# Optimization experiments

Hardware: AMD Instinct MI355X
Metric: run time of the kernel (lower is better)

Reference implementation:

```python
import jax, jax.numpy as jnp
import numpy as np

B, N, M = 2, 2048, 2048
Q_DIM = 1024
HEADS = 8
DIM_HEAD = 64
INNER = HEADS * DIM_HEAD  # 512


def setup_inputs() -> dict:
    key = jax.random.key(0)
    ks = jax.random.split(key, 7)
    s_in = 1.0 / np.sqrt(Q_DIM)
    s_out = 1.0 / np.sqrt(INNER)
    return {
        "x": jax.random.normal(ks[0], (B, N, Q_DIM), dtype=jnp.float32),
        "context": jax.random.normal(ks[1], (B, M, Q_DIM), dtype=jnp.float32),
        "Wq": jax.random.normal(ks[2], (Q_DIM, INNER), dtype=jnp.float32) * s_in,
        "Wk": jax.random.normal(ks[3], (Q_DIM, INNER), dtype=jnp.float32) * s_in,
        "Wv": jax.random.normal(ks[4], (Q_DIM, INNER), dtype=jnp.float32) * s_in,
        "Wo": jax.random.normal(ks[5], (INNER, Q_DIM), dtype=jnp.float32) * s_out,
        "bo": jax.random.normal(ks[6], (Q_DIM,), dtype=jnp.float32) * 0.01,
    }


def reference(x, context, Wq, Wk, Wv, Wo, bo):
    scale = DIM_HEAD ** (-0.5)
    # projections, split heads: [b, n, inner] -> [b, h, n, d]
    def split_heads(t):
        b, n, _ = t.shape
        return t.reshape(b, n, HEADS, DIM_HEAD).transpose(0, 2, 1, 3)
    q = split_heads(x @ Wq)
    k = split_heads(context @ Wk)
    v = split_heads(context @ Wv)
    sim = jnp.einsum('bhid,bhjd->bhij', q, k) * scale  # [b,h,n,m] full score matrix
    attn = jax.nn.softmax(sim, axis=-1)
    out = jnp.einsum('bhij,bhjd->bhid', attn, v)       # [b,h,n,d]
    out = out.transpose(0, 2, 1, 3).reshape(x.shape[0], x.shape[1], INNER)
    return out @ Wo + bo
```

## Files before the change

kernel.cpp:

```cpp
#include <hip/hip_runtime.h>

typedef __attribute__((ext_vector_type(8))) short short8;
typedef __attribute__((ext_vector_type(4))) short bf16x4;
typedef __attribute__((ext_vector_type(4))) float floatx4;
typedef __attribute__((ext_vector_type(4))) float f32x4;

__device__ __forceinline__ short f2bf(float f) {
    union { float f; unsigned u; } v;
    v.f = f;
    unsigned r = v.u + 0x7fffu + ((v.u >> 16) & 1u);
    return (short)(r >> 16);
}
__device__ __forceinline__ short8 cvt8(f32x4 a, f32x4 b) {
    short8 r;
    r[0] = f2bf(a[0]); r[1] = f2bf(a[1]); r[2] = f2bf(a[2]); r[3] = f2bf(a[3]);
    r[4] = f2bf(b[0]); r[5] = f2bf(b[1]); r[6] = f2bf(b[2]); r[7] = f2bf(b[3]);
    return r;
}
__device__ __forceinline__ bf16x4 pack4(float a, float b, float c, float d) {
    union { float f; unsigned u; } x;
    unsigned ua, ub, uc, ud;
    x.f = a; ua = (x.u + 0x8000u) >> 16;
    x.f = b; ub = (x.u + 0x8000u) >> 16;
    x.f = c; uc = (x.u + 0x8000u) >> 16;
    x.f = d; ud = (x.u + 0x8000u) >> 16;
    union { bf16x4 s; unsigned u2[2]; } r;
    r.u2[0] = ua | (ub << 16);
    r.u2[1] = uc | (ud << 16);
    return r.s;
}

#define MFMA_BF16(a, b, c) __builtin_amdgcn_mfma_f32_16x16x32_bf16((a), (b), (c), 0, 0, 0)

__device__ __forceinline__ floatx4 mfma16(bf16x4 a, bf16x4 b, floatx4 c) {
#if __has_builtin(__builtin_amdgcn_mfma_f32_16x16x16bf16_1k)
    return __builtin_amdgcn_mfma_f32_16x16x16bf16_1k(a, b, c, 0, 0, 0);
#else
    floatx4 d;
    asm volatile("v_mfma_f32_16x16x16_bf16 %0, %1, %2, %3"
                 : "=&v"(d) : "v"(a), "v"(b), "v"(c));
    return d;
#endif
}

__device__ __forceinline__ float fast_exp2(float x) {
#if __has_builtin(__builtin_amdgcn_exp2f)
    return __builtin_amdgcn_exp2f(x);
#else
    return exp2f(x);
#endif
}

#define QSCALE_LOG2E 0.18033688011112042f

__global__ __launch_bounds__(256) void cvt_f32_bf16(const float* __restrict__ x,
                                                    const float* __restrict__ ctx,
                                                    short* __restrict__ xb,
                                                    short* __restrict__ ctxb) {
    const size_t i = ((size_t)blockIdx.x * 256 + threadIdx.x) * 8;
    const size_t NT = (size_t)4096 * 1024;
    const float* src = (i < NT) ? x : ctx;
    short* dst = (i < NT) ? xb : ctxb;
    const size_t j = (i < NT) ? i : i - NT;
    f32x4 a = *(const f32x4*)(src + j);
    f32x4 b = *(const f32x4*)(src + j + 4);
    *(short8*)(dst + j) = cvt8(a, b);
}

__global__ __launch_bounds__(256) void transpose_all(const float* __restrict__ Wq,
                                                     const float* __restrict__ Wk,
                                                     const float* __restrict__ Wv,
                                                     const float* __restrict__ Wo,
                                                     short* __restrict__ WqT,
                                                     short* __restrict__ WkT,
                                                     short* __restrict__ WvT,
                                                     short* __restrict__ WoT) {
    const int z = blockIdx.z;
    const float* src = (z == 0) ? Wq : (z == 1) ? Wk : (z == 2) ? Wv : Wo;
    short* dst = (z == 0) ? WqT : (z == 1) ? WkT : (z == 2) ? WvT : WoT;
    const int R = (z < 3) ? 1024 : 512;
    const int C = (z < 3) ? 512 : 1024;
    const int c0 = blockIdx.x * 32;
    const int r0 = blockIdx.y * 32;
    if (c0 >= C || r0 >= R) return;
    __shared__ float tile[32][33];
    const int tx = threadIdx.x;
    const int ty = threadIdx.y;
#pragma unroll
    for (int i = 0; i < 32; i += 8)
        tile[ty + i][tx] = src[(r0 + ty + i) * C + c0 + tx];
    __syncthreads();
#pragma unroll
    for (int i = 0; i < 32; i += 8)
        dst[(c0 + ty + i) * R + r0 + tx] = f2bf(tile[tx][ty + i]);
}

__global__ __launch_bounds__(256, 4) void gemm_qkv(const short* __restrict__ xb,
                                                   const short* __restrict__ ctxb,
                                                   const short* __restrict__ WqT,
                                                   const short* __restrict__ WkT,
                                                   const short* __restrict__ WvT,
                                                   short* __restrict__ Qw,
                                                   short* __restrict__ Kw,
                                                   short* __restrict__ Vtw) {
    const int z = blockIdx.z;
    const short* A  = (z == 0) ? xb : ctxb;
    const short* WT = (z == 0) ? WqT : (z == 1) ? WkT : WvT;
    const int tid = threadIdx.x;
    const int w = tid >> 6;
    const int lane = tid & 63;
    const int quad = lane >> 4, ln = lane & 15;
    const int wr = w >> 1, wc = w & 1;
    const int row0 = blockIdx.x * 64;
    const int col0 = blockIdx.y * 128;

    __shared__ __align__(16) short Alds[2][64][32];
    __shared__ __align__(16) short Blds[2][128][32];

    const int srow = tid >> 2;
    const int scol = (tid & 3) * 8;
    const short* aG = A + (size_t)(row0 + srow) * 1024 + scol;
    const short* bG0 = WT + (size_t)(col0 + srow) * 1024 + scol;
    const short* bG1 = WT + (size_t)(col0 + srow + 64) * 1024 + scol;

    floatx4 acc[2][4] = {};

    {
        *(short8*)(&Alds[0][srow][scol]) = *(const short8*)(aG);
        *(short8*)(&Blds[0][srow][scol]) = *(const short8*)(bG0);
        *(short8*)(&Blds[0][srow + 64][scol]) = *(const short8*)(bG1);
    }
    __syncthreads();

    const int nsteps = 1024 / 32;
    for (int it = 0; it < nsteps; ++it) {
        short8 ar, br0, br1;
        const bool more = (it + 1 < nsteps);
        if (more) {
            const int kk = (it + 1) * 32;
            ar  = *(const short8*)(aG + kk);
            br0 = *(const short8*)(bG0 + kk);
            br1 = *(const short8*)(bG1 + kk);
        }
        const int b = it & 1;
        short8 af[2], bf4[4];
#pragma unroll
        for (int i = 0; i < 2; ++i)
            af[i] = *(const short8*)(&Alds[b][wr * 32 + i * 16 + ln][quad * 8]);
#pragma unroll
        for (int t = 0; t < 4; ++t)
            bf4[t] = *(const short8*)(&Blds[b][wc * 64 + t * 16 + ln][quad * 8]);
#pragma unroll
        for (int i = 0; i < 2; ++i)
#pragma unroll
            for (int t = 0; t < 4; ++t)
                acc[i][t] = MFMA_BF16(af[i], bf4[t], acc[i][t]);
        if (more) {
            const int nb = (it + 1) & 1;
            *(short8*)(&Alds[nb][srow][scol]) = ar;
            *(short8*)(&Blds[nb][srow][scol]) = br0;
            *(short8*)(&Blds[nb][srow + 64][scol]) = br1;
        }
        __syncthreads();
    }

    const float oscale = (z == 0) ? QSCALE_LOG2E : 1.0f;
    short* dst = (z == 0) ? Qw : (z == 1) ? Kw : Vtw;
#pragma unroll
    for (int i = 0; i < 2; ++i)
#pragma unroll
        for (int t = 0; t < 4; ++t)
#pragma unroll
            for (int r = 0; r < 4; ++r) {
                const int R = row0 + wr * 32 + i * 16 + quad * 4 + r;
                const int C = col0 + wc * 64 + t * 16 + ln;
                const int b = R >> 11, n = R & 2047;
                const int h = C >> 6, d = C & 63;
                const short val = f2bf(acc[i][t][r] * oscale);
                if (z < 2)
                    dst[((b * 8 + h) * 2048 + n) * 64 + d] = val;
                else
                    dst[((b * 8 + h) * 64 + d) * 2048 + n] = val;
            }
}

__global__ __launch_bounds__(256, 3) void attn_kernel(const short* __restrict__ Q,
                                                      const short* __restrict__ K,
                                                      const short* __restrict__ Vt,
                                                      float* __restrict__ Opart,
                                                      float* __restrict__ lbuf,
                                                      int chunkLen) {
    const int tid = threadIdx.x;
    const int w = tid >> 6;
    const int lane = tid & 63;
    const int quad = lane >> 4;
    const int ln = lane & 15;
    const int q0 = blockIdx.x * 64;
    const int bh = blockIdx.y;
    const int c = blockIdx.z;

    __shared__ __align__(16) short klds[2][64][72];
    __shared__ __align__(16) short vlds[2][64][72];

    const short* Qbh = Q + bh * 2048 * 64;
    const short* Kbh = K + bh * 2048 * 64;
    const short* Vbh = Vt + bh * 64 * 2048;

    short8 qf[2];
    {
        const int qrow = q0 + w * 16 + ln;
        qf[0] = *(const short8*)(Qbh + qrow * 64 + quad * 8);
        qf[1] = *(const short8*)(Qbh + qrow * 64 + 32 + quad * 8);
    }

    floatx4 ot[4] = {};
    float lp = 0.f;

    const int sr = tid >> 3;
    const int sc = (tid & 7) * 8;

    auto computeTile = [&](int b) {
        short8 kf[8];
#pragma unroll
        for (int t = 0; t < 4; ++t)
#pragma unroll
            for (int ks = 0; ks < 2; ++ks)
                kf[t * 2 + ks] = *(const short8*)(&klds[b][t * 16 + ln][ks * 32 + quad * 8]);
        bf16x4 vf[16];
#pragma unroll
        for (int dt = 0; dt < 4; ++dt)
#pragma unroll
            for (int t = 0; t < 4; ++t)
                vf[dt * 4 + t] = *(const bf16x4*)(&vlds[b][dt * 16 + ln][t * 16 + quad * 4]);

        floatx4 s[4] = {};
#pragma unroll
        for (int ks = 0; ks < 2; ++ks)
#pragma unroll
            for (int t = 0; t < 4; ++t)
                s[t] = MFMA_BF16(kf[t * 2 + ks], qf[ks], s[t]);

        bf16x4 pf[4];
#pragma unroll
        for (int t = 0; t < 4; ++t) {
            float p0 = fast_exp2(s[t][0]);
            float p1 = fast_exp2(s[t][1]);
            float p2 = fast_exp2(s[t][2]);
            float p3 = fast_exp2(s[t][3]);
            lp += (p0 + p1) + (p2 + p3);
            pf[t] = pack4(p0, p1, p2, p3);
        }
#pragma unroll
        for (int t = 0; t < 4; ++t)
#pragma unroll
            for (int dt = 0; dt < 4; ++dt)
                ot[dt] = mfma16(vf[dt * 4 + t], pf[t], ot[dt]);
    };

    const int j0s = c * chunkLen;
    const int nt = chunkLen >> 6;

    {
        short8 k0 = *(const short8*)(Kbh + j0s * 64 + tid * 8);
        short8 k1 = *(const short8*)(Kbh + j0s * 64 + (tid + 256) * 8);
        short8 v0 = *(const short8*)(Vbh + sr * 2048 + j0s + sc);
        short8 v1 = *(const short8*)(Vbh + (sr + 32) * 2048 + j0s + sc);
        *(short8*)(&klds[0][sr][sc]) = k0;
        *(short8*)(&klds[0][sr + 32][sc]) = k1;
        *(short8*)(&vlds[0][sr][sc]) = v0;
        *(short8*)(&vlds[0][sr + 32][sc]) = v1;
    }
    __syncthreads();

    for (int it = 0; it < nt; ++it) {
        short8 k0, k1, v0, v1;
        const bool more = (it + 1 < nt);
        if (more) {
            const int jn = j0s + (it + 1) * 64;
            k0 = *(const short8*)(Kbh + jn * 64 + tid * 8);
            k1 = *(const short8*)(Kbh + jn * 64 + (tid + 256) * 8);
            v0 = *(const short8*)(Vbh + sr * 2048 + jn + sc);
            v1 = *(const short8*)(Vbh + (sr + 32) * 2048 + jn + sc);
        }
        computeTile(it & 1);
        if (more) {
            const int nb = (it + 1) & 1;
            *(short8*)(&klds[nb][sr][sc]) = k0;
            *(short8*)(&klds[nb][sr + 32][sc]) = k1;
            *(short8*)(&vlds[nb][sr][sc]) = v0;
            *(short8*)(&vlds[nb][sr + 32][sc]) = v1;
        }
        __syncthreads();
    }

    lp += __shfl_xor(lp, 16);
    lp += __shfl_xor(lp, 32);

    const int n = q0 + w * 16 + ln;
    float* obase = Opart + (((size_t)(c * 16 + bh) * 2048 + n) * 64) + quad * 4;
#pragma unroll
    for (int dt = 0; dt < 4; ++dt)
        *(f32x4*)(obase + dt * 16) = ot[dt];
    if (quad == 0)
        lbuf[(size_t)(c * 16 + bh) * 2048 + n] = lp;
}

__global__ __launch_bounds__(256) void combine_kernel(const float* __restrict__ Opart,
                                                      const float* __restrict__ lbuf,
                                                      short* __restrict__ Aw,
                                                      int nchunks) {
    const int d = threadIdx.x;
    const int rid = blockIdx.x * 4 + threadIdx.y;
    const int bh = rid >> 11, n = rid & 2047;

    float L = 0.f, O = 0.f;
    for (int c = 0; c < nchunks; ++c) {
        L += lbuf[(size_t)(c * 16 + bh) * 2048 + n];
        O += Opart[(((size_t)(c * 16 + bh) * 2048 + n) * 64) + d];
    }
    const int b = bh >> 3, h = bh & 7;
    Aw[((size_t)(b * 2048 + n) * 512) + h * 64 + d] = f2bf(O / L);
}

__global__ __launch_bounds__(256, 4) void gemm_final(const short* __restrict__ A,
                                                     const short* __restrict__ WoT,
                                                     const float* __restrict__ bias,
                                                     float* __restrict__ out) {
    const int tid = threadIdx.x;
    const int w = tid >> 6;
    const int lane = tid & 63;
    const int quad = lane >> 4, ln = lane & 15;
    const int wr = w >> 1, wc = w & 1;
    const int row0 = blockIdx.x * 64;
    const int col0 = blockIdx.y * 128;

    __shared__ __align__(16) short Alds[2][64][32];
    __shared__ __align__(16) short Blds[2][128][32];

    const int srow = tid >> 2;
    const int scol = (tid & 3) * 8;
    const short* aG = A + (size_t)(row0 + srow) * 512 + scol;
    const short* bG0 = WoT + (size_t)(col0 + srow) * 512 + scol;
    const short* bG1 = WoT + (size_t)(col0 + srow + 64) * 512 + scol;

    floatx4 acc[2][4] = {};

    {
        *(short8*)(&Alds[0][srow][scol]) = *(const short8*)(aG);
        *(short8*)(&Blds[0][srow][scol]) = *(const short8*)(bG0);
        *(short8*)(&Blds[0][srow + 64][scol]) = *(const short8*)(bG1);
    }
    __syncthreads();

    const int nsteps = 512 / 32;
    for (int it = 0; it < nsteps; ++it) {
        short8 ar, br0, br1;
        const bool more = (it + 1 < nsteps);
        if (more) {
            const int kk = (it + 1) * 32;
            ar  = *(const short8*)(aG + kk);
            br0 = *(const short8*)(bG0 + kk);
            br1 = *(const short8*)(bG1 + kk);
        }
        const int b = it & 1;
        short8 af[2], bf4[4];
#pragma unroll
        for (int i = 0; i < 2; ++i)
            af[i] = *(const short8*)(&Alds[b][wr * 32 + i * 16 + ln][quad * 8]);
#pragma unroll
        for (int t = 0; t < 4; ++t)
            bf4[t] = *(const short8*)(&Blds[b][wc * 64 + t * 16 + ln][quad * 8]);
#pragma unroll
        for (int i = 0; i < 2; ++i)
#pragma unroll
            for (int t = 0; t < 4; ++t)
                acc[i][t] = MFMA_BF16(af[i], bf4[t], acc[i][t]);
        if (more) {
            const int nb = (it + 1) & 1;
            *(short8*)(&Alds[nb][srow][scol]) = ar;
            *(short8*)(&Blds[nb][srow][scol]) = br0;
            *(short8*)(&Blds[nb][srow + 64][scol]) = br1;
        }
        __syncthreads();
    }

#pragma unroll
    for (int i = 0; i < 2; ++i)
#pragma unroll
        for (int t = 0; t < 4; ++t)
#pragma unroll
            for (int r = 0; r < 4; ++r) {
                const int R = row0 + wr * 32 + i * 16 + quad * 4 + r;
                const int C = col0 + wc * 64 + t * 16 + ln;
                out[(size_t)R * 1024 + C] = acc[i][t][r] + bias[C];
            }
}

extern "C" void kernel_launch(void* const* d_in, const int* in_sizes, int n_in,
                              void* d_out, int out_size, void* d_ws, size_t ws_size,
                              hipStream_t stream) {
    const float* x   = (const float*)d_in[0];
    const float* ctx = (const float*)d_in[1];
    const float* Wq  = (const float*)d_in[2];
    const float* Wk  = (const float*)d_in[3];
    const float* Wv  = (const float*)d_in[4];
    const float* Wo  = (const float*)d_in[5];
    const float* bo  = (const float*)d_in[6];
    float* out = (float*)d_out;

    char* ws = (char*)d_ws;
    size_t off = 0;
    auto alloc = [&](size_t bytes) { char* p = ws + off; off += (bytes + 255) & ~(size_t)255; return p; };

    short* WqT  = (short*)alloc(512 * 1024 * 2);
    short* WkT  = (short*)alloc(512 * 1024 * 2);
    short* WvT  = (short*)alloc(512 * 1024 * 2);
    short* WoT  = (short*)alloc(1024 * 512 * 2);
    short* xb   = (short*)alloc((size_t)4096 * 1024 * 2);
    short* ctxb = (short*)alloc((size_t)4096 * 1024 * 2);
    short* Qw   = (short*)alloc((size_t)16 * 2048 * 64 * 2);
    short* Kw   = (short*)alloc((size_t)16 * 2048 * 64 * 2);
    short* Vtw  = (short*)alloc((size_t)16 * 2048 * 64 * 2);
    short* Aw   = (short*)alloc((size_t)4096 * 512 * 2);
    size_t base = off;
    const size_t perchunk = (size_t)16 * 2048 * 64 * 4 + (size_t)16 * 2048 * 4 + 512;
    int nchunks = 4;
    while (nchunks > 1 && base + (size_t)nchunks * perchunk > ws_size) nchunks >>= 1;
    float* Opart = (float*)alloc((size_t)nchunks * 16 * 2048 * 64 * 4);
    float* lbuf  = (float*)alloc((size_t)nchunks * 16 * 2048 * 4);
    const int chunkLen = 2048 / nchunks;

    cvt_f32_bf16<<<4096, 256, 0, stream>>>(x, ctx, xb, ctxb);
    transpose_all<<<dim3(32, 32, 4), dim3(32, 8), 0, stream>>>(Wq, Wk, Wv, Wo, WqT, WkT, WvT, WoT);

    gemm_qkv<<<dim3(64, 4, 3), 256, 0, stream>>>(xb, ctxb, WqT, WkT, WvT, Qw, Kw, Vtw);

    attn_kernel<<<dim3(32, 16, nchunks), 256, 0, stream>>>(Qw, Kw, Vtw, Opart, lbuf, chunkLen);
    combine_kernel<<<dim3(8192), dim3(64, 4), 0, stream>>>(Opart, lbuf, Aw, nchunks);

    gemm_final<<<dim3(64, 8), 256, 0, stream>>>(Aw, WoT, bo, out);
}
```

Before: 178.0 us.

## Fuse input bf16 conversion into QKV GEMM and drop split-K attention combine

The standalone fp32-to-bf16 conversion kernel is removed. The QKV GEMM now loads fp32 activations directly and converts them while staging tiles into LDS. The attention kernel no longer splits the key dimension into chunks. Each block processes all 2048 keys, normalises by the row sum and writes bf16 output directly, which removes the fp32 partial buffers and the combine kernel. In exchange the attention grid shrinks from 512×nchunks blocks to 512, which lowers parallelism, and the GEMM reads twice the A bytes per tile and does extra conversion ALU work.

```diff
diff --git a/kernel.cpp b/kernel.cpp
--- a/kernel.cpp
+++ b/kernel.cpp
@@ -52,20 +52,6 @@
 }
 
 #define QSCALE_LOG2E 0.18033688011112042f
-
-__global__ __launch_bounds__(256) void cvt_f32_bf16(const float* __restrict__ x,
-                                                    const float* __restrict__ ctx,
-                                                    short* __restrict__ xb,
-                                                    short* __restrict__ ctxb) {
-    const size_t i = ((size_t)blockIdx.x * 256 + threadIdx.x) * 8;
-    const size_t NT = (size_t)4096 * 1024;
-    const float* src = (i < NT) ? x : ctx;
-    short* dst = (i < NT) ? xb : ctxb;
-    const size_t j = (i < NT) ? i : i - NT;
-    f32x4 a = *(const f32x4*)(src + j);
-    f32x4 b = *(const f32x4*)(src + j + 4);
-    *(short8*)(dst + j) = cvt8(a, b);
-}
 
 __global__ __launch_bounds__(256) void transpose_all(const float* __restrict__ Wq,
                                                      const float* __restrict__ Wk,
@@ -95,8 +81,8 @@
         dst[(c0 + ty + i) * R + r0 + tx] = f2bf(tile[tx][ty + i]);
 }
 
-__global__ __launch_bounds__(256, 4) void gemm_qkv(const short* __restrict__ xb,
-                                                   const short* __restrict__ ctxb,
+__global__ __launch_bounds__(256, 4) void gemm_qkv(const float* __restrict__ x,
+                                                   const float* __restrict__ ctx,
                                                    const short* __restrict__ WqT,
                                                    const short* __restrict__ WkT,
                                                    const short* __restrict__ WvT,
@@ -104,7 +90,7 @@
                                                    short* __restrict__ Kw,
                                                    short* __restrict__ Vtw) {
     const int z = blockIdx.z;
-    const short* A  = (z == 0) ? xb : ctxb;
+    const float* A  = (z == 0) ? x : ctx;
     const short* WT = (z == 0) ? WqT : (z == 1) ? WkT : WvT;
     const int tid = threadIdx.x;
     const int w = tid >> 6;
@@ -119,14 +105,16 @@
 
     const int srow = tid >> 2;
     const int scol = (tid & 3) * 8;
-    const short* aG = A + (size_t)(row0 + srow) * 1024 + scol;
+    const float* aG = A + (size_t)(row0 + srow) * 1024 + scol;
     const short* bG0 = WT + (size_t)(col0 + srow) * 1024 + scol;
     const short* bG1 = WT + (size_t)(col0 + srow + 64) * 1024 + scol;
 
     floatx4 acc[2][4] = {};
 
     {
-        *(short8*)(&Alds[0][srow][scol]) = *(const short8*)(aG);
+        f32x4 a0 = *(const f32x4*)(aG);
+        f32x4 a1 = *(const f32x4*)(aG + 4);
+        *(short8*)(&Alds[0][srow][scol]) = cvt8(a0, a1);
         *(short8*)(&Blds[0][srow][scol]) = *(const short8*)(bG0);
         *(short8*)(&Blds[0][srow + 64][scol]) = *(const short8*)(bG1);
     }
@@ -134,11 +122,13 @@
 
     const int nsteps = 1024 / 32;
     for (int it = 0; it < nsteps; ++it) {
-        short8 ar, br0, br1;
+        f32x4 a0, a1;
+        short8 br0, br1;
         const bool more = (it + 1 < nsteps);
         if (more) {
             const int kk = (it + 1) * 32;
-            ar  = *(const short8*)(aG + kk);
+            a0  = *(const f32x4*)(aG + kk);
+            a1  = *(const f32x4*)(aG + kk + 4);
             br0 = *(const short8*)(bG0 + kk);
             br1 = *(const short8*)(bG1 + kk);
         }
@@ -157,7 +147,7 @@
                 acc[i][t] = MFMA_BF16(af[i], bf4[t], acc[i][t]);
         if (more) {
             const int nb = (it + 1) & 1;
-            *(short8*)(&Alds[nb][srow][scol]) = ar;
+            *(short8*)(&Alds[nb][srow][scol]) = cvt8(a0, a1);
             *(short8*)(&Blds[nb][srow][scol]) = br0;
             *(short8*)(&Blds[nb][srow + 64][scol]) = br1;
         }
@@ -184,12 +174,10 @@
             }
 }
 
-__global__ __launch_bounds__(256, 3) void attn_kernel(const short* __restrict__ Q,
+__global__ __launch_bounds__(256, 2) void attn_kernel(const short* __restrict__ Q,
                                                       const short* __restrict__ K,
                                                       const short* __restrict__ Vt,
-                                                      float* __restrict__ Opart,
-                                                      float* __restrict__ lbuf,
-                                                      int chunkLen) {
+                                                      short* __restrict__ Aw) {
     const int tid = threadIdx.x;
     const int w = tid >> 6;
     const int lane = tid & 63;
@@ -197,7 +185,6 @@
     const int ln = lane & 15;
     const int q0 = blockIdx.x * 64;
     const int bh = blockIdx.y;
-    const int c = blockIdx.z;
 
     __shared__ __align__(16) short klds[2][64][72];
     __shared__ __align__(16) short vlds[2][64][72];
@@ -257,14 +244,13 @@
                 ot[dt] = mfma16(vf[dt * 4 + t], pf[t], ot[dt]);
     };
 
-    const int j0s = c * chunkLen;
-    const int nt = chunkLen >> 6;
+    const int nt = 2048 / 64;
 
     {
-        short8 k0 = *(const short8*)(Kbh + j0s * 64 + tid * 8);
-        short8 k1 = *(const short8*)(Kbh + j0s * 64 + (tid + 256) * 8);
-        short8 v0 = *(const short8*)(Vbh + sr * 2048 + j0s + sc);
-        short8 v1 = *(const short8*)(Vbh + (sr + 32) * 2048 + j0s + sc);
+        short8 k0 = *(const short8*)(Kbh + tid * 8);
+        short8 k1 = *(const short8*)(Kbh + (tid + 256) * 8);
+        short8 v0 = *(const short8*)(Vbh + sr * 2048 + sc);
+        short8 v1 = *(const short8*)(Vbh + (sr + 32) * 2048 + sc);
         *(short8*)(&klds[0][sr][sc]) = k0;
         *(short8*)(&klds[0][sr + 32][sc]) = k1;
         *(short8*)(&vlds[0][sr][sc]) = v0;
@@ -276,7 +262,7 @@
         short8 k0, k1, v0, v1;
         const bool more = (it + 1 < nt);
         if (more) {
-            const int jn = j0s + (it + 1) * 64;
+            const int jn = (it + 1) * 64;
             k0 = *(const short8*)(Kbh + jn * 64 + tid * 8);
             k1 = *(const short8*)(Kbh + jn * 64 + (tid + 256) * 8);
             v0 = *(const short8*)(Vbh + sr * 2048 + jn + sc);
@@ -295,31 +281,15 @@
 
     lp += __shfl_xor(lp, 16);
     lp += __shfl_xor(lp, 32);
+    const float invL = 1.0f / lp;
 
     const int n = q0 + w * 16 + ln;
-    float* obase = Opart + (((size_t)(c * 16 + bh) * 2048 + n) * 64) + quad * 4;
+    const int b = bh >> 3, h = bh & 7;
+    short* abase = Aw + ((size_t)(b * 2048 + n) * 512) + h * 64 + quad * 4;
 #pragma unroll
     for (int dt = 0; dt < 4; ++dt)
-        *(f32x4*)(obase + dt * 16) = ot[dt];
-    if (quad == 0)
-        lbuf[(size_t)(c * 16 + bh) * 2048 + n] = lp;
-}
-
-__global__ __launch_bounds__(256) void combine_kernel(const float* __restrict__ Opart,
-                                                      const float* __restrict__ lbuf,
-                                                      short* __restrict__ Aw,
-                                                      int nchunks) {
-    const int d = threadIdx.x;
-    const int rid = blockIdx.x * 4 + threadIdx.y;
-    const int bh = rid >> 11, n = rid & 2047;
-
-    float L = 0.f, O = 0.f;
-    for (int c = 0; c < nchunks; ++c) {
-        L += lbuf[(size_t)(c * 16 + bh) * 2048 + n];
-        O += Opart[(((size_t)(c * 16 + bh) * 2048 + n) * 64) + d];
-    }
-    const int b = bh >> 3, h = bh & 7;
-    Aw[((size_t)(b * 2048 + n) * 512) + h * 64 + d] = f2bf(O / L);
+        *(bf16x4*)(abase + dt * 16) =
+            pack4(ot[dt][0] * invL, ot[dt][1] * invL, ot[dt][2] * invL, ot[dt][3] * invL);
 }
 
 __global__ __launch_bounds__(256, 4) void gemm_final(const short* __restrict__ A,
@@ -416,27 +386,16 @@
     short* WkT  = (short*)alloc(512 * 1024 * 2);
     short* WvT  = (short*)alloc(512 * 1024 * 2);
     short* WoT  = (short*)alloc(1024 * 512 * 2);
-    short* xb   = (short*)alloc((size_t)4096 * 1024 * 2);
-    short* ctxb = (short*)alloc((size_t)4096 * 1024 * 2);
     short* Qw   = (short*)alloc((size_t)16 * 2048 * 64 * 2);
     short* Kw   = (short*)alloc((size_t)16 * 2048 * 64 * 2);
     short* Vtw  = (short*)alloc((size_t)16 * 2048 * 64 * 2);
     short* Aw   = (short*)alloc((size_t)4096 * 512 * 2);
-    size_t base = off;
-    const size_t perchunk = (size_t)16 * 2048 * 64 * 4 + (size_t)16 * 2048 * 4 + 512;
-    int nchunks = 4;
-    while (nchunks > 1 && base + (size_t)nchunks * perchunk > ws_size) nchunks >>= 1;
-    float* Opart = (float*)alloc((size_t)nchunks * 16 * 2048 * 64 * 4);
-    float* lbuf  = (float*)alloc((size_t)nchunks * 16 * 2048 * 4);
-    const int chunkLen = 2048 / nchunks;
-
-    cvt_f32_bf16<<<4096, 256, 0, stream>>>(x, ctx, xb, ctxb);
+
     transpose_all<<<dim3(32, 32, 4), dim3(32, 8), 0, stream>>>(Wq, Wk, Wv, Wo, WqT, WkT, WvT, WoT);
 
-    gemm_qkv<<<dim3(64, 4, 3), 256, 0, stream>>>(xb, ctxb, WqT, WkT, WvT, Qw, Kw, Vtw);
-
-    attn_kernel<<<dim3(32, 16, nchunks), 256, 0, stream>>>(Qw, Kw, Vtw, Opart, lbuf, chunkLen);
-    combine_kernel<<<dim3(8192), dim3(64, 4), 0, stream>>>(Opart, lbuf, Aw, nchunks);
+    gemm_qkv<<<dim3(64, 4, 3), 256, 0, stream>>>(x, ctx, WqT, WkT, WvT, Qw, Kw, Vtw);
+
+    attn_kernel<<<dim3(32, 16), 256, 0, stream>>>(Qw, Kw, Vtw, Aw);
 
     gemm_final<<<dim3(64, 8), 256, 0, stream>>>(Aw, WoT, bo, out);
 }
```

After: 171.8 us. 3.5% less time.
